# Optimization experiments

Measured on AMD Instinct MI355X. Metric: run time of the kernel, lower is better.

Reference implementation:

```python
import jax, jax.numpy as jnp
import numpy as np


def setup_inputs() -> dict:
    key = jax.random.key(0)
    k1, k2 = jax.random.split(key)
    B, T, D, K = 16, 1024, 256, 8192
    x = jax.random.normal(k1, (B, T, D), dtype=jnp.float32)
    # mimic nn.Embedding init uniform_(-1/K, 1/K)
    codebook = jax.random.uniform(k2, (K, D), dtype=jnp.float32,
                                  minval=-1.0 / K, maxval=1.0 / K)
    return {"x": x, "codebook": codebook}


def reference(x, codebook):
    sg = jax.lax.stop_gradient
    x2 = jnp.sum(x * x, axis=-1, keepdims=True)               # [B, T, 1]
    c2 = jnp.sum(codebook * codebook, axis=-1)                # [K]
    xc = jnp.einsum('btd,kd->btk', x, codebook)               # [B, T, K]
    dist2 = x2 - 2.0 * xc + c2                                # [B, T, K]
    indices = jnp.argmin(dist2, axis=-1)                      # [B, T] int
    cb_vecs = codebook[indices]                               # [B, T, D]
    # straight-through estimator
    quantized = x + sg(cb_vecs - x)
    codebook_loss = jnp.mean((quantized - sg(x)) ** 2)
    commitment_loss = jnp.mean((sg(quantized) - x) ** 2)
    quantize_loss = codebook_loss + commitment_loss
    return (quantized, indices, quantize_loss)
```

## Files before the change

### kernel.cpp

```cpp
#include <hip/hip_runtime.h>
#include <float.h>

typedef __attribute__((ext_vector_type(8))) short short8;
typedef __attribute__((ext_vector_type(4))) float f32x4;

#define BT    16384
#define DM    256
#define KC    8192
#define QOFF  (BT * DM)
#define LOFF  (QOFF + BT)
#define MARGIN 2e-4f

#define E_XH 0
#define E_CH (BT * DM)
#define WS_BF16_BYTES ((size_t)(BT * DM + KC * DM) * 2)
#define WS_SLOT_OFF   WS_BF16_BYTES
#define WS_SLOT_BYTES ((size_t)64 * BT * 8)
#define WS_LP_OFF     (WS_SLOT_OFF + WS_SLOT_BYTES)
#define WS_NEED       (WS_LP_OFF + 4096 * 4)


__device__ inline ushort bf16rne(float f) {
    unsigned u = __float_as_uint(f);
    return (ushort)((u + 0x7FFFu + ((u >> 16) & 1u)) >> 16);
}
__device__ inline unsigned umax2(unsigned a, unsigned b) { return a > b ? a : b; }
__device__ inline unsigned umin2(unsigned a, unsigned b) { return a < b ? a : b; }

__device__ __forceinline__ void gl_lds16(const void* g, void* l) {
    __builtin_amdgcn_global_load_lds(
        (const __attribute__((address_space(1))) void*)g,
        (__attribute__((address_space(3))) void*)l, 16, 0, 0);
}

__global__ __launch_bounds__(256) void k_cvt(const float* __restrict__ x,
                                             const float* __restrict__ cb,
                                             ushort* __restrict__ ws) {
    const int XN = BT * DM / 4;
    const int CN = KC * DM / 4;
    int idx = blockIdx.x * 256 + threadIdx.x;
    const float4* src;
    ushort* dh; int o;
    if (idx < XN) { src = (const float4*)x; dh = ws + E_XH; o = idx; }
    else {
        o = idx - XN;
        if (o >= CN) return;
        src = (const float4*)cb; dh = ws + E_CH;
    }
    float4 v = src[o];
    ushort4 h;
    h.x = bf16rne(v.x);
    h.y = bf16rne(v.y);
    h.z = bf16rne(v.z);
    h.w = bf16rne(v.w);
    ((ushort4*)dh)[o] = h;
}

__global__ __launch_bounds__(256, 2) void k_main_mfma(const ushort* __restrict__ ws,
                                                      uint2* __restrict__ slotb) {
    __shared__ ushort sTok[2][64 * 256];
    __shared__ uint2  msc[2][2][64];

    const int tid = threadIdx.x;
    const int w = tid >> 6, L = tid & 63;
    const int lq = L >> 4, lr = L & 15;
    const int wm = w >> 1, wn = w & 1;
    const int grp   = blockIdx.x >> 3;
    const int chunk = blockIdx.x & 7;
    const int c0    = grp * 128 + wm * 64;
    const int tok0  = chunk * 2048;
    const unsigned lw = ((unsigned)wm << 6) | ((unsigned)lq << 2);

    const short8* ch8 = (const short8*)(ws + E_CH);
    const uint4*  xh4 = (const uint4*)(ws + E_XH);

    short8 a[4][8];
    #pragma unroll
    for (int i = 0; i < 4; ++i)
        #pragma unroll
        for (int ks = 0; ks < 8; ++ks)
            a[i][ks] = ch8[(size_t)(c0 + i * 16 + lr) * 32 + ks * 4 + lq];

    const int half = L >> 5;
    const int g32  = L & 31;

    {
        const uint4* src = xh4 + (size_t)(tok0 + w * 16) * 32;
        #pragma unroll
        for (int q = 0; q < 8; ++q) {
            int rrel = 2 * q + half;
            int sg   = g32 ^ (rrel & 7);
            gl_lds16(src + (size_t)rrel * 32 + sg,
                     &sTok[0][(w * 16 + 2 * q) * 256]);
        }
    }
    __syncthreads();

    const int mtl = wn * 32 + wm * 16 + lr;

    for (int p = 0; p < 32; ++p) {
        const int cur = p & 1;

        if (p + 1 < 32) {
            const uint4* src = xh4 + (size_t)(tok0 + (p + 1) * 64 + w * 16) * 32;
            #pragma unroll
            for (int q = 0; q < 8; ++q) {
                int rrel = 2 * q + half;
                int sg   = g32 ^ (rrel & 7);
                gl_lds16(src + (size_t)rrel * 32 + sg,
                         &sTok[cur ^ 1][(w * 16 + 2 * q) * 256]);
            }
        }

        f32x4 acc[4][2];
        #pragma unroll
        for (int i = 0; i < 4; ++i)
            #pragma unroll
            for (int j = 0; j < 2; ++j)
                acc[i][j] = (f32x4){0.25f, 0.25f, 0.25f, 0.25f};

        const ushort* tb = &sTok[cur][0];
        #pragma unroll
        for (int ks = 0; ks < 8; ++ks) {
            short8 b[2];
            #pragma unroll
            for (int j = 0; j < 2; ++j) {
                int row = wn * 32 + j * 16 + lr;
                b[j] = *(const short8*)(tb + row * 256 + (((ks * 4 + lq) ^ (lr & 7)) * 8));
            }
            #pragma unroll
            for (int i = 0; i < 4; ++i)
                #pragma unroll
                for (int j = 0; j < 2; ++j)
                    acc[i][j] = __builtin_amdgcn_mfma_f32_16x16x32_bf16(a[i][ks], b[j], acc[i][j], 0, 0, 0);
        }

        #pragma unroll
        for (int j = 0; j < 2; ++j) {
            unsigned h[8], l[8];
            #pragma unroll
            for (int i = 0; i < 4; ++i)
                #pragma unroll
                for (int rp = 0; rp < 2; ++rp) {
                    unsigned e0 = (__float_as_uint(acc[i][j][2 * rp])     & 0xFFFFFF80u) | lw | (i << 4) | (2 * rp);
                    unsigned e1 = (__float_as_uint(acc[i][j][2 * rp + 1]) & 0xFFFFFF80u) | lw | (i << 4) | (2 * rp + 1);
                    h[i * 2 + rp] = umax2(e0, e1);
                    l[i * 2 + rp] = umin2(e0, e1);
                }
            #pragma unroll
            for (int s = 4; s >= 1; s >>= 1)
                #pragma unroll
                for (int q = 0; q < 4; ++q) {
                    if (q < s) {
                        unsigned H = umax2(h[q], h[q + s]);
                        unsigned m = umin2(h[q], h[q + s]);
                        l[q] = umax2(m, umax2(l[q], l[q + s]));
                        h[q] = H;
                    }
                }
            unsigned H = h[0], L2 = l[0];
            #pragma unroll
            for (int off = 16; off <= 32; off <<= 1) {
                unsigned oH = (unsigned)__shfl_xor((int)H, off);
                unsigned oL = (unsigned)__shfl_xor((int)L2, off);
                unsigned m = umin2(H, oH);
                H = umax2(H, oH);
                L2 = umax2(m, umax2(L2, oL));
            }
            if (lq == 0)
                msc[cur][wm][wn * 32 + j * 16 + lr] = make_uint2(H, L2);
        }

        if (p >= 1 && lq == 0) {
            uint2 A = msc[cur ^ 1][0][mtl];
            uint2 B = msc[cur ^ 1][1][mtl];
            unsigned H = umax2(A.x, B.x);
            unsigned m = umin2(A.x, B.x);
            unsigned L2 = umax2(m, umax2(A.y, B.y));
            int token = tok0 + (p - 1) * 64 + mtl;
            slotb[(size_t)grp * BT + token] = make_uint2(H, L2);
        }

        __syncthreads();
    }

    if (lq == 0) {
        uint2 A = msc[1][0][mtl];
        uint2 B = msc[1][1][mtl];
        unsigned H = umax2(A.x, B.x);
        unsigned m = umin2(A.x, B.x);
        unsigned L2 = umax2(m, umax2(A.y, B.y));
        int token = tok0 + 31 * 64 + mtl;
        slotb[(size_t)grp * BT + token] = make_uint2(H, L2);
    }
}

__global__ __launch_bounds__(256) void k_gather(const float* __restrict__ x,
                                                const float* __restrict__ cb,
                                                const uint2* __restrict__ slotb,
                                                float* __restrict__ out,
                                                float* __restrict__ lp) {
    __shared__ float4 xls[4][64];
    __shared__ int candk[4][16];
    __shared__ float bsum[4];

    const int w = threadIdx.x >> 6;
    const int L = threadIdx.x & 63;
    const int t = blockIdx.x * 4 + w;

    const float4 xv = ((const float4*)x)[(size_t)t * 64 + L];
    xls[w][L] = xv;

    const uint2 s = slotb[(size_t)L * BT + t];
    float v1 = __uint_as_float(s.x & 0xFFFFFF80u);
    float v2 = __uint_as_float(s.y & 0xFFFFFF80u);
    int   k1 = L * 128 + (int)(s.x & 127u);
    int   k2 = L * 128 + (int)(s.y & 127u);

    float lm = v1; int lk = k1;
    #pragma unroll
    for (int off = 32; off; off >>= 1) {
        float ov = __shfl_xor(lm, off);
        int   ok = __shfl_xor(lk, off);
        if (ov > lm || (ov == lm && ok < lk)) { lm = ov; lk = ok; }
    }
    const float thr = lm - MARGIN;

    int* ct = candk[w];
    if (L == 0) ct[0] = lk;
    int ncand = 1;
    #pragma unroll
    for (int ph = 0; ph < 2; ++ph) {
        float vv = ph ? v2 : v1;
        int   kf = ph ? k2 : k1;
        unsigned long long bal = __ballot(vv >= thr);
        while (bal) {
            int src = __ffsll(bal) - 1;
            bal &= bal - 1;
            int kv = __shfl(kf, src);
            if (L == 0 && ncand < 16) ct[ncand] = kv;
            ncand++;
        }
    }
    if (ncand > 16) ncand = 16;

    int best;
    if (ncand <= 1) {
        best = lk;
    } else {
        double dl = (double)xv.x * xv.x + (double)xv.y * xv.y
                  + (double)xv.z * xv.z + (double)xv.w * xv.w;
        #pragma unroll
        for (int off = 32; off; off >>= 1) dl += __shfl_xor(dl, off);
        const float x2 = (float)dl;

        const int g = L >> 2, l4 = L & 3;
        float sex = FLT_MAX;
        int   kk  = 0x7fffffff;
        if (g < ncand) {
            kk = ct[g];
            const float* xr = (const float*)&xls[w][0];
            const float* cr = cb + (size_t)kk * DM;
            float acc = 0.f;
            {
#pragma clang fp contract(off)
                #pragma unroll 8
                for (int m = 0; m < 64; m++) {
                    float p2 = xr[4 * m + l4] * cr[4 * m + l4];
                    acc = acc + p2;
                }
            }
            float t1 = acc + __shfl_xor(acc, 1);
            float xc = t1 + __shfl_xor(t1, 2);
            sex = x2 - 2.0f * xc;
        }
        #pragma unroll
        for (int off = 32; off; off >>= 1) {
            float os = __shfl_xor(sex, off);
            int   ok = __shfl_xor(kk, off);
            if (os < sex || (os == sex && ok < kk)) { sex = os; kk = ok; }
        }
        best = kk;
    }

    const float4 cv = ((const float4*)cb)[(size_t)best * 64 + L];
    float4 e, q;
    e.x = cv.x - xv.x; q.x = xv.x + e.x;
    e.y = cv.y - xv.y; q.y = xv.y + e.y;
    e.z = cv.z - xv.z; q.z = xv.z + e.z;
    e.w = cv.w - xv.w; q.w = xv.w + e.w;
    ((float4*)out)[(size_t)t * 64 + L] = q;
    if (L == 0) out[QOFF + t] = (float)best;

    float ls = e.x * e.x + e.y * e.y + e.z * e.z + e.w * e.w;
    #pragma unroll
    for (int off = 32; off; off >>= 1) ls += __shfl_xor(ls, off);
    if (L == 0) bsum[w] = ls;
    __syncthreads();
    if (threadIdx.x == 0)
        lp[blockIdx.x] = bsum[0] + bsum[1] + bsum[2] + bsum[3];
}


#define TM    64
#define TK    64
#define NSPLIT 2
#define KPS   (KC / NSPLIT)
#define LDSW  68

__global__ __launch_bounds__(256, 2) void k_main_f32(const float* __restrict__ x,
                                                     const float* __restrict__ cb,
                                                     float* __restrict__ out) {
    __shared__ float xs[TM * LDSW];
    __shared__ float cs[TK * LDSW];

    const int tid = threadIdx.x;
    const int ty = tid >> 4, tx = tid & 15;
    const int split = blockIdx.x & 1;
    const int tb    = blockIdx.x >> 1;
    const int t0    = tb * TM;
    const int kb0   = split * KPS;
    const int txc   = tx & 7;
    const int srow = tid >> 4;
    const int sc4  = tid & 15;
    const float4* x4  = (const float4*)x;
    const float4* cb4 = (const float4*)cb;

    float mv[4][4];
    int   mi[4][4];
    #pragma unroll
    for (int i = 0; i < 4; i++)
        #pragma unroll
        for (int j = 0; j < 4; j++) { mv[i][j] = -FLT_MAX; mi[i][j] = 0; }

    for (int k0 = 0; k0 < KPS; k0 += TK) {
        float dot[4][4];
        #pragma unroll
        for (int i = 0; i < 4; i++)
            #pragma unroll
            for (int j = 0; j < 4; j++) dot[i][j] = 0.f;

        for (int d0 = 0; d0 < DM; d0 += 64) {
            __syncthreads();
            const int d04 = d0 >> 2;
            #pragma unroll
            for (int r = 0; r < 4; r++) {
                int row = srow + 16 * r;
                float4 xv = x4[(size_t)(t0 + row) * 64 + d04 + sc4];
                *(float4*)&xs[row * LDSW + sc4 * 4] = xv;
                int gc = sc4 ^ ((row >> 2) & 7);
                float4 cv = cb4[(size_t)(kb0 + k0 + row) * 64 + d04 + gc];
                *(float4*)&cs[row * LDSW + sc4 * 4] = cv;
            }
            __syncthreads();

            #pragma unroll
            for (int u = 0; u < 16; u++) {
                float4 xa[4];
                #pragma unroll
                for (int i = 0; i < 4; i++)
                    xa[i] = *(const float4*)&xs[(ty * 4 + i) * LDSW + u * 4];
                const int ww = u ^ txc;
                float4 cv[4];
                #pragma unroll
                for (int j = 0; j < 4; j++)
                    cv[j] = *(const float4*)&cs[(tx * 4 + j) * LDSW + ww * 4];
                #pragma unroll
                for (int i = 0; i < 4; i++)
                    #pragma unroll
                    for (int j = 0; j < 4; j++) {
                        dot[i][j] = fmaf(xa[i].x, cv[j].x, dot[i][j]);
                        dot[i][j] = fmaf(xa[i].y, cv[j].y, dot[i][j]);
                        dot[i][j] = fmaf(xa[i].z, cv[j].z, dot[i][j]);
                        dot[i][j] = fmaf(xa[i].w, cv[j].w, dot[i][j]);
                    }
            }
        }

        const int kk0 = kb0 + k0 + tx * 4;
        #pragma unroll
        for (int i = 0; i < 4; i++)
            #pragma unroll
            for (int j = 0; j < 4; j++) {
                float d = dot[i][j];
                int   kk = kk0 + j;
                if (d > mv[i][3]) {
                    if (d > mv[i][1]) {
                        if (d > mv[i][0]) {
                            mv[i][3]=mv[i][2]; mi[i][3]=mi[i][2];
                            mv[i][2]=mv[i][1]; mi[i][2]=mi[i][1];
                            mv[i][1]=mv[i][0]; mi[i][1]=mi[i][0];
                            mv[i][0]=d;        mi[i][0]=kk;
                        } else {
                            mv[i][3]=mv[i][2]; mi[i][3]=mi[i][2];
                            mv[i][2]=mv[i][1]; mi[i][2]=mi[i][1];
                            mv[i][1]=d;        mi[i][1]=kk;
                        }
                    } else {
                        if (d > mv[i][2]) {
                            mv[i][3]=mv[i][2]; mi[i][3]=mi[i][2];
                            mv[i][2]=d;        mi[i][2]=kk;
                        } else {
                            mv[i][3]=d;        mi[i][3]=kk;
                        }
                    }
                }
            }
    }

    #pragma unroll
    for (int i = 0; i < 4; i++) {
        int t = t0 + ty * 4 + i;
        float4 v4 = { mv[i][0], mv[i][1], mv[i][2], mv[i][3] };
        float4 k4 = { (float)mi[i][0], (float)mi[i][1], (float)mi[i][2], (float)mi[i][3] };
        float4* dst = (float4*)(out + (size_t)t * DM + (split * 16 + tx) * 8);
        dst[0] = v4;
        dst[1] = k4;
    }
}

__global__ __launch_bounds__(256) void k_gather_f32(const float* __restrict__ x,
                                                    const float* __restrict__ cb,
                                                    float* __restrict__ out,
                                                    float* __restrict__ lp) {
    __shared__ float4 xls[4][64];
    __shared__ int candk[4][20];
    __shared__ float bsum[4];

    const int w = threadIdx.x >> 6;
    const int L = threadIdx.x & 63;
    const int t = blockIdx.x * 4 + w;

    const float4 xv = ((const float4*)x)[(size_t)t * 64 + L];
    xls[w][L] = xv;
    const float4 f = ((const float4*)(out + (size_t)t * DM))[L];
    const bool even = ((L & 1) == 0);

    double dl = (double)xv.x * xv.x + (double)xv.y * xv.y
              + (double)xv.z * xv.z + (double)xv.w * xv.w;
    #pragma unroll
    for (int off = 32; off; off >>= 1) dl += __shfl_xor(dl, off);
    const float x2 = (float)dl;

    float lm = even ? fmaxf(fmaxf(f.x, f.y), fmaxf(f.z, f.w)) : -FLT_MAX;
    #pragma unroll
    for (int off = 32; off; off >>= 1) lm = fmaxf(lm, __shfl_xor(lm, off));
    const float thr = lm - 5e-5f;

    int ncand = 0;
    #pragma unroll
    for (int j = 0; j < 4; j++) {
        float vj = (j == 0) ? f.x : (j == 1) ? f.y : (j == 2) ? f.z : f.w;
        bool flag = even && (vj >= thr);
        unsigned long long bal = __ballot(flag);
        while (bal) {
            int src = __ffsll(bal) - 1;
            bal &= bal - 1;
            float kv = __shfl(vj, src + 1);
            if (L == 0 && ncand < 20) candk[w][ncand] = (int)kv;
            ncand++;
        }
    }
    if (ncand > 16) ncand = 16;

    int best;
    if (ncand == 1) {
        best = candk[w][0];
    } else {
        const int g = L >> 2, l4 = L & 3;
        float sex = FLT_MAX;
        int   kk  = 0x7fffffff;
        if (g < ncand) {
            kk = candk[w][g];
            const float* xr = (const float*)&xls[w][0];
            const float* cr = cb + (size_t)kk * DM;
            float acc = 0.f;
            {
#pragma clang fp contract(off)
                #pragma unroll 8
                for (int m = 0; m < 64; m++) {
                    float p = xr[4 * m + l4] * cr[4 * m + l4];
                    acc = acc + p;
                }
            }
            float t1 = acc + __shfl_xor(acc, 1);
            float xc = t1 + __shfl_xor(t1, 2);
            sex = x2 - 2.0f * xc;
        }
        #pragma unroll
        for (int off = 32; off; off >>= 1) {
            float os = __shfl_xor(sex, off);
            int   ok = __shfl_xor(kk, off);
            if (os < sex || (os == sex && ok < kk)) { sex = os; kk = ok; }
        }
        best = kk;
    }

    const float4 cv = ((const float4*)cb)[(size_t)best * 64 + L];
    float4 e, q;
    e.x = cv.x - xv.x; q.x = xv.x + e.x;
    e.y = cv.y - xv.y; q.y = xv.y + e.y;
    e.z = cv.z - xv.z; q.z = xv.z + e.z;
    e.w = cv.w - xv.w; q.w = xv.w + e.w;
    ((float4*)out)[(size_t)t * 64 + L] = q;
    if (L == 0) out[QOFF + t] = (float)best;

    float ls = e.x * e.x + e.y * e.y + e.z * e.z + e.w * e.w;
    #pragma unroll
    for (int off = 32; off; off >>= 1) ls += __shfl_xor(ls, off);
    if (L == 0) bsum[w] = ls;
    __syncthreads();
    if (threadIdx.x == 0)
        lp[blockIdx.x] = bsum[0] + bsum[1] + bsum[2] + bsum[3];
}

__global__ __launch_bounds__(256) void k_loss(const float* __restrict__ lp,
                                              float* __restrict__ out) {
    __shared__ double sd[256];
    double s = 0.0;
    for (int i = threadIdx.x; i < BT / 4; i += 256) s += (double)lp[i];
    sd[threadIdx.x] = s;
    __syncthreads();
    for (int st = 128; st; st >>= 1) {
        if (threadIdx.x < st) sd[threadIdx.x] += sd[threadIdx.x + st];
        __syncthreads();
    }
    if (threadIdx.x == 0)
        out[LOFF] = (float)(2.0 * sd[0] / (double)QOFF);
}

extern "C" void kernel_launch(void* const* d_in, const int* in_sizes, int n_in,
                              void* d_out, int out_size, void* d_ws, size_t ws_size,
                              hipStream_t stream) {
    const float* x  = (const float*)d_in[0];
    const float* cb = (const float*)d_in[1];
    float* out = (float*)d_out;

    if (ws_size >= (size_t)WS_NEED) {
        ushort* wsu   = (ushort*)d_ws;
        uint2*  slotb = (uint2*)((char*)d_ws + WS_SLOT_OFF);
        float*  lp    = (float*)((char*)d_ws + WS_LP_OFF);
        k_cvt      <<<6144, 256, 0, stream>>>(x, cb, wsu);
        k_main_mfma<<<512,  256, 0, stream>>>(wsu, slotb);
        k_gather   <<<BT / 4, 256, 0, stream>>>(x, cb, slotb, out, lp);
        k_loss     <<<1,    256, 0, stream>>>(lp, out);
    } else {
        float* lp = (float*)d_ws;
        k_main_f32  <<<(BT / TM) * NSPLIT, 256, 0, stream>>>(x, cb, out);
        k_gather_f32<<<BT / 4,             256, 0, stream>>>(x, cb, out, lp);
        k_loss      <<<1,                  256, 0, stream>>>(lp, out);
    }
}
```

Before: 107.4 us.

## Software-pipeline MFMA panels with deferred fold of previous accumulator

Restructures the distance-matmul main loop into a two-stage software pipeline with two accumulator sets. Each panel's MFMAs are issued before the previous panel's bitwise top-2 fold and cross-wave merge, so the scalar/VALU reduction work can overlap with matrix-core work. MFMA sections are also wrapped in s_setprio to raise wave priority while issuing matrix ops. The cost is a second set of accumulator registers, which may raise VGPR pressure and reduce occupancy.

```diff
diff --git a/kernel.cpp b/kernel.cpp
--- a/kernel.cpp
+++ b/kernel.cpp
@@ -83,58 +83,43 @@
 
     const int half = L >> 5;
     const int g32  = L & 31;
-
-    {
-        const uint4* src = xh4 + (size_t)(tok0 + w * 16) * 32;
+    const int mtl  = wn * 32 + wm * 16 + lr;
+    const int sw   = lr & 7;
+
+    auto DMA = [&](int p) {
+        const uint4* src = xh4 + (size_t)(tok0 + p * 64 + w * 16) * 32;
         #pragma unroll
         for (int q = 0; q < 8; ++q) {
             int rrel = 2 * q + half;
-            int sg   = g32 ^ (rrel & 7);
-            gl_lds16(src + (size_t)rrel * 32 + sg,
-                     &sTok[0][(w * 16 + 2 * q) * 256]);
-        }
-    }
-    __syncthreads();
-
-    const int mtl = wn * 32 + wm * 16 + lr;
-
-    for (int p = 0; p < 32; ++p) {
-        const int cur = p & 1;
-
-        if (p + 1 < 32) {
-            const uint4* src = xh4 + (size_t)(tok0 + (p + 1) * 64 + w * 16) * 32;
-            #pragma unroll
-            for (int q = 0; q < 8; ++q) {
-                int rrel = 2 * q + half;
-                int sg   = g32 ^ (rrel & 7);
-                gl_lds16(src + (size_t)rrel * 32 + sg,
-                         &sTok[cur ^ 1][(w * 16 + 2 * q) * 256]);
-            }
-        }
-
-        f32x4 acc[4][2];
+            gl_lds16(src + (size_t)rrel * 32 + (g32 ^ (rrel & 7)),
+                     &sTok[p & 1][(w * 16 + 2 * q) * 256]);
+        }
+    };
+
+    auto MFMA_PANEL = [&](f32x4 (&acc)[4][2], const ushort* tb) {
         #pragma unroll
         for (int i = 0; i < 4; ++i)
             #pragma unroll
             for (int j = 0; j < 2; ++j)
                 acc[i][j] = (f32x4){0.25f, 0.25f, 0.25f, 0.25f};
-
-        const ushort* tb = &sTok[cur][0];
+        const ushort* rp0 = tb + (wn * 32 + lr) * 256;
+        const ushort* rp1 = tb + (wn * 32 + 16 + lr) * 256;
+        __builtin_amdgcn_s_setprio(1);
         #pragma unroll
         for (int ks = 0; ks < 8; ++ks) {
-            short8 b[2];
-            #pragma unroll
-            for (int j = 0; j < 2; ++j) {
-                int row = wn * 32 + j * 16 + lr;
-                b[j] = *(const short8*)(tb + row * 256 + (((ks * 4 + lq) ^ (lr & 7)) * 8));
-            }
-            #pragma unroll
-            for (int i = 0; i < 4; ++i)
-                #pragma unroll
-                for (int j = 0; j < 2; ++j)
-                    acc[i][j] = __builtin_amdgcn_mfma_f32_16x16x32_bf16(a[i][ks], b[j], acc[i][j], 0, 0, 0);
-        }
-
+            int g = ((ks * 4 + lq) ^ sw) * 8;
+            short8 b0 = *(const short8*)(rp0 + g);
+            short8 b1 = *(const short8*)(rp1 + g);
+            #pragma unroll
+            for (int i = 0; i < 4; ++i) {
+                acc[i][0] = __builtin_amdgcn_mfma_f32_16x16x32_bf16(a[i][ks], b0, acc[i][0], 0, 0, 0);
+                acc[i][1] = __builtin_amdgcn_mfma_f32_16x16x32_bf16(a[i][ks], b1, acc[i][1], 0, 0, 0);
+            }
+        }
+        __builtin_amdgcn_s_setprio(0);
+    };
+
+    auto FOLD = [&](const f32x4 (&acc)[4][2], int mbuf) {
         #pragma unroll
         for (int j = 0; j < 2; ++j) {
             unsigned h[8], l[8];
@@ -168,31 +153,45 @@
                 L2 = umax2(m, umax2(L2, oL));
             }
             if (lq == 0)
-                msc[cur][wm][wn * 32 + j * 16 + lr] = make_uint2(H, L2);
-        }
-
-        if (p >= 1 && lq == 0) {
-            uint2 A = msc[cur ^ 1][0][mtl];
-            uint2 B = msc[cur ^ 1][1][mtl];
+                msc[mbuf][wm][wn * 32 + j * 16 + lr] = make_uint2(H, L2);
+        }
+    };
+
+    auto MERGE = [&](int p, int mbuf) {
+        if (lq == 0) {
+            uint2 A = msc[mbuf][0][mtl];
+            uint2 B = msc[mbuf][1][mtl];
             unsigned H = umax2(A.x, B.x);
             unsigned m = umin2(A.x, B.x);
             unsigned L2 = umax2(m, umax2(A.y, B.y));
-            int token = tok0 + (p - 1) * 64 + mtl;
-            slotb[(size_t)grp * BT + token] = make_uint2(H, L2);
-        }
-
+            slotb[(size_t)grp * BT + tok0 + p * 64 + mtl] = make_uint2(H, L2);
+        }
+    };
+
+    DMA(0);
+    __syncthreads();
+
+    f32x4 accA[4][2], accB[4][2];
+
+    for (int t = 0; t < 16; ++t) {
+        const int pe = 2 * t;
+        DMA(pe + 1);
+        MFMA_PANEL(accA, &sTok[0][0]);
+        if (t >= 1) FOLD(accB, 1);
+        if (t >= 1) MERGE(pe - 2, 0);
         __syncthreads();
-    }
-
-    if (lq == 0) {
-        uint2 A = msc[1][0][mtl];
-        uint2 B = msc[1][1][mtl];
-        unsigned H = umax2(A.x, B.x);
-        unsigned m = umin2(A.x, B.x);
-        unsigned L2 = umax2(m, umax2(A.y, B.y));
-        int token = tok0 + 31 * 64 + mtl;
-        slotb[(size_t)grp * BT + token] = make_uint2(H, L2);
-    }
+
+        if (t < 15) DMA(pe + 2);
+        MFMA_PANEL(accB, &sTok[1][0]);
+        FOLD(accA, 0);
+        if (t >= 1) MERGE(pe - 1, 1);
+        __syncthreads();
+    }
+
+    FOLD(accB, 1);
+    MERGE(30, 0);
+    __syncthreads();
+    MERGE(31, 1);
 }
 
 __global__ __launch_bounds__(256) void k_gather(const float* __restrict__ x,
```

New measurement: 143.3 us. 33.5% more time.
